# Performance work log

Hardware: AMD Instinct MI355X
Metric: run time of the kernel (lower is better)

## Reference

```python
import jax, jax.numpy as jnp
import numpy as np

IN_F = 1024
OUT_F = 1024
INT_DIM = 128


def setup_inputs() -> dict:
    key = jax.random.key(0)
    k_x, k_wc, k_bc, k_pw, k_pb = jax.random.split(key, 5)
    # coef init per init_kaiming_uniform: fan_in = in_features, gain for
    # leaky_relu(a=sqrt(5)) = sqrt(2/(1+5)) = sqrt(1/3)
    fan_in = IN_F
    gain = np.sqrt(2.0 / (1.0 + 5.0))
    out_std = gain / np.sqrt(fan_in)
    w_bound = np.sqrt(3.0) * np.sqrt(3.0 / INT_DIM) * out_std
    b_bound = w_bound  # same int_dim and out_std for bias coef
    x = jax.random.normal(k_x, (8, 2048, IN_F), dtype=jnp.float32)
    weight_coef = jax.random.uniform(k_wc, (INT_DIM,), jnp.float32, -w_bound, w_bound)
    bias_coef = jax.random.uniform(k_bc, (INT_DIM,), jnp.float32, -b_bound, b_bound)
    # fixed (seed-determined, non-learned) random projection bases
    P_w = jax.random.normal(k_pw, (INT_DIM, OUT_F * IN_F), dtype=jnp.float32)
    P_b = jax.random.normal(k_pb, (INT_DIM, OUT_F), dtype=jnp.float32)
    return {"x": x, "weight_coef": weight_coef, "bias_coef": bias_coef,
            "P_w": P_w, "P_b": P_b}


def reference(x, weight_coef, bias_coef, P_w, P_b):
    # Expand low-dim coefs through the fixed random projection into the
    # full weight/bias (RandumbTensor materialization), then F.linear.
    W = (weight_coef @ P_w).reshape(OUT_F, IN_F)   # [out, in]
    b = bias_coef @ P_b                            # [out]
    # y = x A^T + b
    return jnp.einsum('bsi,oi->bso', x, W) + b
```

## Files before the change

### kernel.cpp

```cpp
#include <hip/hip_runtime.h>
#include <stdint.h>

#define IN_F 1024
#define OUT_F 1024
#define INT_DIM 128
#define M_ROWS 16384

#define BM 128
#define BN 128
#define BK 32

typedef float f32x4 __attribute__((ext_vector_type(4)));
typedef __bf16 bf16x8 __attribute__((ext_vector_type(8)));

__device__ __forceinline__ unsigned short f2bf(float f) {
  unsigned int u = __float_as_uint(f);
  u += 0x7fffu + ((u >> 16) & 1u);
  return (unsigned short)(u >> 16);
}

__device__ __forceinline__ void async_copy16(void* lds_dst, const void* gsrc) {
  __builtin_amdgcn_global_load_lds(
      (const __attribute__((address_space(1))) void*)gsrc,
      (__attribute__((address_space(3))) void*)lds_dst, 16, 0, 0);
}

__global__ void expand_w_kernel(const float* __restrict__ coef,
                                const float* __restrict__ Pw,
                                unsigned short* __restrict__ W) {
  __shared__ float c[INT_DIM];
  if (threadIdx.x < INT_DIM) c[threadIdx.x] = coef[threadIdx.x];
  __syncthreads();
  const int j4 = blockIdx.x * 256 + threadIdx.x;
  const float4* P4 = (const float4*)Pw;
  float4 acc = make_float4(0.f, 0.f, 0.f, 0.f);
#pragma unroll 8
  for (int d = 0; d < INT_DIM; ++d) {
    float4 p = P4[(size_t)d * (OUT_F * IN_F / 4) + j4];
    float cd = c[d];
    acc.x += cd * p.x;
    acc.y += cd * p.y;
    acc.z += cd * p.z;
    acc.w += cd * p.w;
  }
  union { unsigned short us[4]; uint2 u; } o;
  o.us[0] = f2bf(acc.x);
  o.us[1] = f2bf(acc.y);
  o.us[2] = f2bf(acc.z);
  o.us[3] = f2bf(acc.w);
  ((uint2*)W)[j4] = o.u;
}

__global__ void expand_b_kernel(const float* __restrict__ coef,
                                const float* __restrict__ Pb,
                                float* __restrict__ bias) {
  const int o = blockIdx.x * 256 + threadIdx.x;
  float acc = 0.f;
#pragma unroll 8
  for (int d = 0; d < INT_DIM; ++d) acc += coef[d] * Pb[d * OUT_F + o];
  bias[o] = acc;
}

__global__ __launch_bounds__(256) void gemm_xf32_bt_kernel(
    const float* __restrict__ A,
    const unsigned short* __restrict__ B,
    const float* __restrict__ bias,
    float* __restrict__ C) {
  constexpr int K = IN_F;
  constexpr int N = OUT_F;
  __shared__ float sA[BM * BK];
  __shared__ unsigned short sB[BN * BK];

  const int tid = threadIdx.x;
  const int bm = blockIdx.x * BM;
  const int bn = blockIdx.y * BN;
  const int lane = tid & 63;
  const int wave = tid >> 6;
  const int wm = (wave >> 1) * 64;
  const int wn = (wave & 1) * 64;
  const int lm = lane & 15;
  const int quad = lane >> 4;

  const float* aSrc[4];
#pragma unroll
  for (int j = 0; j < 4; ++j) {
    const int d = tid + 256 * j;
    const int rd = d >> 3;
    const int cd = d & 7;
    aSrc[j] = A + (size_t)(bm + rd) * K + ((cd ^ (rd & 7)) << 2);
  }

  const int q0 = tid;
  const int q1 = tid + 256;
  const int r0 = q0 >> 2, kc0 = (q0 & 3) * 8;
  const int r1 = q1 >> 2, kc1 = (q1 & 3) * 8;

  const int sw = lm & 7;
  const int co0 = (((quad << 1) | 0) ^ sw) << 2;
  const int co1 = (((quad << 1) | 1) ^ sw) << 2;

  f32x4 acc[4][4];
  const f32x4 zero = {0.f, 0.f, 0.f, 0.f};
#pragma unroll
  for (int i = 0; i < 4; ++i)
#pragma unroll
    for (int j = 0; j < 4; ++j) acc[i][j] = zero;

  for (int k0 = 0; k0 < K; k0 += BK) {
#pragma unroll
    for (int j = 0; j < 4; ++j)
      async_copy16(&sA[(tid + 256 * j) * 4], aSrc[j] + k0);
    async_copy16(&sB[q0 * 8], &B[(size_t)(bn + r0) * K + k0 + kc0]);
    async_copy16(&sB[q1 * 8], &B[(size_t)(bn + r1) * K + k0 + kc1]);
    __syncthreads();

    bf16x8 af[4], bfr[4];
#pragma unroll
    for (int f = 0; f < 4; ++f) {
      const int rbase = (wm + f * 16 + lm) * BK;
      const f32x4 lo = *(const f32x4*)&sA[rbase + co0];
      const f32x4 hi = *(const f32x4*)&sA[rbase + co1];
      bf16x8 v;
      v[0] = (__bf16)lo[0]; v[1] = (__bf16)lo[1];
      v[2] = (__bf16)lo[2]; v[3] = (__bf16)lo[3];
      v[4] = (__bf16)hi[0]; v[5] = (__bf16)hi[1];
      v[6] = (__bf16)hi[2]; v[7] = (__bf16)hi[3];
      af[f] = v;
    }
#pragma unroll
    for (int f = 0; f < 4; ++f)
      bfr[f] = *(const bf16x8*)&sB[(wn + f * 16 + lm) * BK + quad * 8];

#pragma unroll
    for (int fm = 0; fm < 4; ++fm)
#pragma unroll
      for (int fn = 0; fn < 4; ++fn)
        acc[fm][fn] = __builtin_amdgcn_mfma_f32_16x16x32_bf16(
            af[fm], bfr[fn], acc[fm][fn], 0, 0, 0);
    __syncthreads();
  }

  float bv[4];
#pragma unroll
  for (int fn = 0; fn < 4; ++fn) bv[fn] = bias[bn + wn + fn * 16 + lm];
#pragma unroll
  for (int fm = 0; fm < 4; ++fm) {
#pragma unroll
    for (int r = 0; r < 4; ++r) {
      const int row = bm + wm + fm * 16 + quad * 4 + r;
      float* crow = C + (size_t)row * N + bn + wn + lm;
#pragma unroll
      for (int fn = 0; fn < 4; ++fn) crow[fn * 16] = acc[fm][fn][r] + bv[fn];
    }
  }
}

extern "C" void kernel_launch(void* const* d_in, const int* in_sizes, int n_in,
                              void* d_out, int out_size, void* d_ws,
                              size_t ws_size, hipStream_t stream) {
  const float* x = (const float*)d_in[0];
  const float* wc = (const float*)d_in[1];
  const float* bc = (const float*)d_in[2];
  const float* Pw = (const float*)d_in[3];
  const float* Pb = (const float*)d_in[4];
  float* out = (float*)d_out;

  unsigned short* W = (unsigned short*)d_ws;
  float* bias = (float*)((char*)d_ws + (2u << 20));

  expand_w_kernel<<<OUT_F * IN_F / 4 / 256, 256, 0, stream>>>(wc, Pw, W);
  expand_b_kernel<<<OUT_F / 256, 256, 0, stream>>>(bc, Pb, bias);

  dim3 grid(M_ROWS / BM, OUT_F / BN);
  gemm_xf32_bt_kernel<<<grid, 256, 0, stream>>>(x, W, bias, out);
}
```

Baseline: 808.0 us.

## Restructure GEMM into double-buffered four-phase pipeline with larger tiles

Rewrites the GEMM kernel to use 512 threads, 128x256x64 tiles, and double-buffered LDS. The K loop is split into four phases, each issuing MFMA quadrants at raised priority while async global-to-LDS copies for the next tiles are in flight. B is now XOR-swizzled in LDS to avoid bank conflicts, and hand-written waitcnt and barrier sequences replace __syncthreads. The goal is to hide global load latency and cut barrier stalls. The cost is higher LDS use (about 192KB for two blocks per CU) and fragile manual synchronisation.

```diff
diff --git a/kernel.cpp b/kernel.cpp
--- a/kernel.cpp
+++ b/kernel.cpp
@@ -7,8 +7,9 @@
 #define M_ROWS 16384
 
 #define BM 128
-#define BN 128
-#define BK 32
+#define BN 256
+#define BK 64
+#define NT (IN_F / BK)
 
 typedef float f32x4 __attribute__((ext_vector_type(4)));
 typedef __bf16 bf16x8 __attribute__((ext_vector_type(8)));
@@ -61,43 +62,89 @@
   bias[o] = acc;
 }
 
-__global__ __launch_bounds__(256) void gemm_xf32_bt_kernel(
+__global__ __launch_bounds__(512, 2) void gemm_4ph_kernel(
     const float* __restrict__ A,
     const unsigned short* __restrict__ B,
     const float* __restrict__ bias,
     float* __restrict__ C) {
   constexpr int K = IN_F;
   constexpr int N = OUT_F;
-  __shared__ float sA[BM * BK];
-  __shared__ unsigned short sB[BN * BK];
+  __shared__ float sA[2][BM * BK];
+  __shared__ unsigned short sB[2][BN * BK];
 
   const int tid = threadIdx.x;
-  const int bm = blockIdx.x * BM;
-  const int bn = blockIdx.y * BN;
+  const int bid = blockIdx.x;
+  const int bm = (bid & 127) * BM;
+  const int bn = (bid >> 7) * BN;
   const int lane = tid & 63;
   const int wave = tid >> 6;
-  const int wm = (wave >> 1) * 64;
-  const int wn = (wave & 1) * 64;
+  const int wr = wave >> 2;
+  const int wc = wave & 3;
   const int lm = lane & 15;
   const int quad = lane >> 4;
-
-  const float* aSrc[4];
-#pragma unroll
-  for (int j = 0; j < 4; ++j) {
-    const int d = tid + 256 * j;
-    const int rd = d >> 3;
-    const int cd = d & 7;
-    aSrc[j] = A + (size_t)(bm + rd) * K + ((cd ^ (rd & 7)) << 2);
-  }
-
-  const int q0 = tid;
-  const int q1 = tid + 256;
-  const int r0 = q0 >> 2, kc0 = (q0 & 3) * 8;
-  const int r1 = q1 >> 2, kc1 = (q1 & 3) * 8;
-
   const int sw = lm & 7;
-  const int co0 = (((quad << 1) | 0) ^ sw) << 2;
-  const int co1 = (((quad << 1) | 1) ^ sw) << 2;
+
+  const float *aS0, *aS1, *aS2, *aS3;
+  int aD0, aD1, aD2, aD3;
+  {
+    int d, rd, cd;
+    d = tid;            rd = d >> 4; cd = d & 15;
+    aS0 = A + (size_t)(bm + rd) * K + ((cd ^ (rd & 7)) << 2); aD0 = d << 2;
+    d = tid + 512;      rd = d >> 4; cd = d & 15;
+    aS1 = A + (size_t)(bm + rd) * K + ((cd ^ (rd & 7)) << 2); aD1 = d << 2;
+    d = tid + 1024;     rd = d >> 4; cd = d & 15;
+    aS2 = A + (size_t)(bm + rd) * K + ((cd ^ (rd & 7)) << 2); aD2 = d << 2;
+    d = tid + 1536;     rd = d >> 4; cd = d & 15;
+    aS3 = A + (size_t)(bm + rd) * K + ((cd ^ (rd & 7)) << 2); aD3 = d << 2;
+  }
+  const unsigned short *bS0, *bS1, *bS2, *bS3;
+  int bD0, bD1, bD2, bD3;
+  {
+    int d, rd, cd;
+    d = tid;            rd = d >> 3; cd = d & 7;
+    bS0 = B + (size_t)(bn + rd) * K + ((cd ^ (rd & 7)) << 3); bD0 = d << 3;
+    d = tid + 512;      rd = d >> 3; cd = d & 7;
+    bS1 = B + (size_t)(bn + rd) * K + ((cd ^ (rd & 7)) << 3); bD1 = d << 3;
+    d = tid + 1024;     rd = d >> 3; cd = d & 7;
+    bS2 = B + (size_t)(bn + rd) * K + ((cd ^ (rd & 7)) << 3); bD2 = d << 3;
+    d = tid + 1536;     rd = d >> 3; cd = d & 7;
+    bS3 = B + (size_t)(bn + rd) * K + ((cd ^ (rd & 7)) << 3); bD3 = d << 3;
+  }
+
+#define STAGE_A(buf, t)                                \
+  do {                                                 \
+    async_copy16(&sA[buf][aD0], aS0 + (t) * BK);       \
+    async_copy16(&sA[buf][aD1], aS1 + (t) * BK);       \
+    async_copy16(&sA[buf][aD2], aS2 + (t) * BK);       \
+    async_copy16(&sA[buf][aD3], aS3 + (t) * BK);       \
+  } while (0)
+#define STAGE_B(buf, t)                                \
+  do {                                                 \
+    async_copy16(&sB[buf][bD0], bS0 + (t) * BK);       \
+    async_copy16(&sB[buf][bD1], bS1 + (t) * BK);       \
+    async_copy16(&sB[buf][bD2], bS2 + (t) * BK);       \
+    async_copy16(&sB[buf][bD3], bS3 + (t) * BK);       \
+  } while (0)
+
+#define PHASE_BAR() \
+  asm volatile("s_waitcnt lgkmcnt(0)\n\ts_barrier" ::: "memory")
+
+  int aOff[2][2];
+#pragma unroll
+  for (int kk = 0; kk < 2; ++kk)
+#pragma unroll
+    for (int h = 0; h < 2; ++h)
+      aOff[kk][h] = ((kk * 8 + quad * 2 + h) ^ sw) << 2;
+  int bOff[2];
+#pragma unroll
+  for (int kk = 0; kk < 2; ++kk)
+    bOff[kk] = ((kk * 4 + quad) ^ sw) << 3;
+  int aRow[4], bRow[4];
+#pragma unroll
+  for (int f = 0; f < 4; ++f) {
+    aRow[f] = (wr * 64 + f * 16 + lm) * BK;
+    bRow[f] = (wc * 64 + f * 16 + lm) * BK;
+  }
 
   f32x4 acc[4][4];
   const f32x4 zero = {0.f, 0.f, 0.f, 0.f};
@@ -106,53 +153,102 @@
 #pragma unroll
     for (int j = 0; j < 4; ++j) acc[i][j] = zero;
 
-  for (int k0 = 0; k0 < K; k0 += BK) {
-#pragma unroll
-    for (int j = 0; j < 4; ++j)
-      async_copy16(&sA[(tid + 256 * j) * 4], aSrc[j] + k0);
-    async_copy16(&sB[q0 * 8], &B[(size_t)(bn + r0) * K + k0 + kc0]);
-    async_copy16(&sB[q1 * 8], &B[(size_t)(bn + r1) * K + k0 + kc1]);
-    __syncthreads();
-
-    bf16x8 af[4], bfr[4];
-#pragma unroll
-    for (int f = 0; f < 4; ++f) {
-      const int rbase = (wm + f * 16 + lm) * BK;
-      const f32x4 lo = *(const f32x4*)&sA[rbase + co0];
-      const f32x4 hi = *(const f32x4*)&sA[rbase + co1];
-      bf16x8 v;
-      v[0] = (__bf16)lo[0]; v[1] = (__bf16)lo[1];
-      v[2] = (__bf16)lo[2]; v[3] = (__bf16)lo[3];
-      v[4] = (__bf16)hi[0]; v[5] = (__bf16)hi[1];
-      v[6] = (__bf16)hi[2]; v[7] = (__bf16)hi[3];
-      af[f] = v;
+  bf16x8 af[2][2];
+  bf16x8 bfr[4][2];
+
+#define READ_A(pA, fmBase)                                              \
+  do {                                                                  \
+    _Pragma("unroll") for (int i = 0; i < 2; ++i) {                     \
+      _Pragma("unroll") for (int kk = 0; kk < 2; ++kk) {                \
+        f32x4 lo = *(const f32x4*)((pA) + aRow[(fmBase) + i] + aOff[kk][0]); \
+        f32x4 hi = *(const f32x4*)((pA) + aRow[(fmBase) + i] + aOff[kk][1]); \
+        bf16x8 v;                                                       \
+        v[0] = (__bf16)lo[0]; v[1] = (__bf16)lo[1];                     \
+        v[2] = (__bf16)lo[2]; v[3] = (__bf16)lo[3];                     \
+        v[4] = (__bf16)hi[0]; v[5] = (__bf16)hi[1];                     \
+        v[6] = (__bf16)hi[2]; v[7] = (__bf16)hi[3];                     \
+        af[i][kk] = v;                                                  \
+      }                                                                 \
+    }                                                                   \
+  } while (0)
+
+#define MFMA_Q(accM, accN)                                              \
+  do {                                                                  \
+    __builtin_amdgcn_s_setprio(1);                                      \
+    _Pragma("unroll") for (int i = 0; i < 2; ++i)                       \
+      _Pragma("unroll") for (int j = 0; j < 2; ++j)                     \
+        _Pragma("unroll") for (int kk = 0; kk < 2; ++kk)                \
+          acc[(accM) + i][(accN) + j] =                                 \
+              __builtin_amdgcn_mfma_f32_16x16x32_bf16(                  \
+                  af[i][kk], bfr[(accN) + j][kk],                       \
+                  acc[(accM) + i][(accN) + j], 0, 0, 0);                \
+    __builtin_amdgcn_s_setprio(0);                                      \
+  } while (0)
+
+  STAGE_A(0, 0);
+  asm volatile("" ::: "memory");
+  STAGE_B(0, 0);
+  asm volatile("" ::: "memory");
+  STAGE_A(1, 1);
+  asm volatile("s_waitcnt vmcnt(4)\n\ts_barrier" ::: "memory");
+
+  int cur = 0;
+  for (int t = 0; t < NT; ++t) {
+    const float* pA = sA[cur];
+    const unsigned short* pB = sB[cur];
+    const int nxt = cur ^ 1;
+
+    READ_A(pA, 0);
+#pragma unroll
+    for (int j = 0; j < 2; ++j)
+#pragma unroll
+      for (int kk = 0; kk < 2; ++kk)
+        bfr[j][kk] = *(const bf16x8*)(pB + bRow[j] + bOff[kk]);
+    MFMA_Q(0, 0);
+    PHASE_BAR();
+
+#pragma unroll
+    for (int j = 2; j < 4; ++j)
+#pragma unroll
+      for (int kk = 0; kk < 2; ++kk)
+        bfr[j][kk] = *(const bf16x8*)(pB + bRow[j] + bOff[kk]);
+    if (t + 1 < NT) STAGE_B(nxt, t + 1);
+    MFMA_Q(0, 2);
+    PHASE_BAR();
+
+    READ_A(pA, 2);
+    MFMA_Q(2, 2);
+    PHASE_BAR();
+
+    if (t + 2 < NT) STAGE_A(cur, t + 2);
+    MFMA_Q(2, 0);
+    if (t + 1 < NT) {
+      if (t + 2 < NT)
+        asm volatile("s_waitcnt vmcnt(4) lgkmcnt(0)\n\ts_barrier" ::: "memory");
+      else
+        asm volatile("s_waitcnt vmcnt(0) lgkmcnt(0)\n\ts_barrier" ::: "memory");
     }
-#pragma unroll
-    for (int f = 0; f < 4; ++f)
-      bfr[f] = *(const bf16x8*)&sB[(wn + f * 16 + lm) * BK + quad * 8];
-
-#pragma unroll
-    for (int fm = 0; fm < 4; ++fm)
-#pragma unroll
-      for (int fn = 0; fn < 4; ++fn)
-        acc[fm][fn] = __builtin_amdgcn_mfma_f32_16x16x32_bf16(
-            af[fm], bfr[fn], acc[fm][fn], 0, 0, 0);
-    __syncthreads();
+    cur = nxt;
   }
 
   float bv[4];
 #pragma unroll
-  for (int fn = 0; fn < 4; ++fn) bv[fn] = bias[bn + wn + fn * 16 + lm];
+  for (int fn = 0; fn < 4; ++fn) bv[fn] = bias[bn + wc * 64 + fn * 16 + lm];
 #pragma unroll
   for (int fm = 0; fm < 4; ++fm) {
 #pragma unroll
     for (int r = 0; r < 4; ++r) {
-      const int row = bm + wm + fm * 16 + quad * 4 + r;
-      float* crow = C + (size_t)row * N + bn + wn + lm;
+      const int row = bm + wr * 64 + fm * 16 + quad * 4 + r;
+      float* crow = C + (size_t)row * N + bn + wc * 64 + lm;
 #pragma unroll
       for (int fn = 0; fn < 4; ++fn) crow[fn * 16] = acc[fm][fn][r] + bv[fn];
     }
   }
+#undef STAGE_A
+#undef STAGE_B
+#undef PHASE_BAR
+#undef READ_A
+#undef MFMA_Q
 }
 
 extern "C" void kernel_launch(void* const* d_in, const int* in_sizes, int n_in,
@@ -171,6 +267,5 @@
   expand_w_kernel<<<OUT_F * IN_F / 4 / 256, 256, 0, stream>>>(wc, Pw, W);
   expand_b_kernel<<<OUT_F / 256, 256, 0, stream>>>(bc, Pb, bias);
 
-  dim3 grid(M_ROWS / BM, OUT_F / BN);
-  gemm_xf32_bt_kernel<<<grid, 256, 0, stream>>>(x, W, bias, out);
-}
+  gemm_4ph_kernel<<<dim3(512), 512, 0, stream>>>(x, W, bias, out);
+}
```

Result: no change. 805.0 us (-0.4%).
